# Performance work log

Measured on AMD Instinct MI355X. Metric: run time of the kernel, lower is better.

The kernel has to match this reference:

```python
import jax, jax.numpy as jnp
import numpy as np

D_MODEL = 1024
HEADS = 16
D_K = D_MODEL // HEADS
SCALE = 1.0 / np.sqrt(D_K)


def setup_inputs() -> dict:
    key = jax.random.key(0)
    ks = jax.random.split(key, 12)
    B, S = 4, 2048
    std = 1.0 / np.sqrt(D_MODEL)
    inp = {
        "query": jax.random.normal(ks[0], (B, S, D_MODEL), jnp.float32),
        "key": jax.random.normal(ks[1], (B, S, D_MODEL), jnp.float32),
        "value": jax.random.normal(ks[2], (B, S, D_MODEL), jnp.float32),
        # projection weights stored [in, out] (transpose of torch Linear)
        "Wq": jax.random.normal(ks[3], (D_MODEL, D_MODEL), jnp.float32) * std,
        "bq": jax.random.normal(ks[4], (D_MODEL,), jnp.float32) * std,
        "Wk": jax.random.normal(ks[5], (D_MODEL, D_MODEL), jnp.float32) * std,
        "bk": jax.random.normal(ks[6], (D_MODEL,), jnp.float32) * std,
        "Wv": jax.random.normal(ks[7], (D_MODEL, D_MODEL), jnp.float32) * std,
        "bv": jax.random.normal(ks[8], (D_MODEL,), jnp.float32) * std,
        "Wo": jax.random.normal(ks[9], (D_MODEL, D_MODEL), jnp.float32) * std,
        "bo": jax.random.normal(ks[10], (D_MODEL,), jnp.float32) * std,
    }
    return inp


def _proj(x, W, b):
    # [B,S,D] -> [B,S,H,Dk]
    B, S, _ = x.shape
    return (x @ W + b).reshape(B, S, HEADS, D_K)


def reference(query, key, value, Wq, bq, Wk, bk, Wv, bv, Wo, bo):
    B, S, _ = query.shape
    Q = _proj(query, Wq, bq)
    K = _proj(key, Wk, bk)
    V = _proj(value, Wv, bv)
    scores = jnp.einsum('bihd,bjhd->bijh', Q, K) * SCALE
    # FAITHFUL to original: nn.Softmax(dim=1) normalizes over the QUERY axis i
    attn = jax.nn.softmax(scores, axis=1)
    # dropout is identity at inference
    x = jnp.einsum('bijh,bjhd->bihd', attn, V).reshape(B, S, D_MODEL)
    return x @ Wo + bo
```

## Files before the change

### kernel.cpp

```cpp
#include <hip/hip_runtime.h>


#define B_   4
#define S_   2048
#define D_   1024
#define H_   16
#define DK_  64
#define BH_  64
#define SC2_    0.18033688f

typedef __bf16 bf16x2 __attribute__((ext_vector_type(2)));
typedef __bf16 bf16x4 __attribute__((ext_vector_type(4)));
typedef __bf16 bf16x8 __attribute__((ext_vector_type(8)));
typedef float  f32x4  __attribute__((ext_vector_type(4)));
typedef unsigned int u32;

#define MFMA16(a,b,c) __builtin_amdgcn_mfma_f32_16x16x32_bf16((a),(b),(c),0,0,0)

__device__ __forceinline__ bf16x8 ld8(const __bf16* p){ return *(const bf16x8*)p; }

__device__ __forceinline__ void gll16(const __bf16* g, __bf16* l) {
    __builtin_amdgcn_global_load_lds(
        (const __attribute__((address_space(1))) u32*)g,
        (__attribute__((address_space(3))) u32*)l, 16, 0, 0);
}

__global__ __launch_bounds__(256) void wtrans3(
    const float* __restrict__ W0, const float* __restrict__ W1,
    const float* __restrict__ W2, __bf16* __restrict__ Wt)
{
    __shared__ __align__(16) __bf16 Ls[64][80];
    const int t = threadIdx.x;
    const int k0 = blockIdx.x * 64, n0 = blockIdx.y * 64, z = blockIdx.z;
    const float* W = (z == 0) ? W0 : ((z == 1) ? W1 : W2);
    __bf16* out = Wt + (size_t)z * D_ * D_;

#pragma unroll
    for (int p = 0; p < 4; ++p) {
        int id = p*256 + t;
        int k = id >> 4, nq = id & 15;
        f32x4 v = *(const f32x4*)&W[(size_t)(k0 + k)*D_ + n0 + nq*4];
#pragma unroll
        for (int u = 0; u < 4; ++u) Ls[nq*4 + u][k] = (__bf16)v[u];
    }
    __syncthreads();
#pragma unroll
    for (int p = 0; p < 2; ++p) {
        int id = p*256 + t;
        int n = id >> 3, c = id & 7;
        *(bf16x8*)&out[(size_t)(n0 + n)*D_ + k0 + c*8] =
            *(const bf16x8*)&Ls[n][c*8];
    }
}

template<int ABF16, int MODE, int QS>
__global__ __launch_bounds__(256) void gemm128(
    const void* __restrict__ Ap, const __bf16* __restrict__ Wt,
    const float* __restrict__ bias, void* __restrict__ C)
{
    __shared__ __align__(16) __bf16 As[128*32];
    __shared__ __align__(16) __bf16 Bs[128*32];

    const int t = threadIdx.x, lane = t & 63, w = t >> 6;
    const int wm = w >> 1, wn = w & 1;
    const int fr = lane & 15, fq = lane >> 4;
    const int gid = blockIdx.x;
    const int m0 = (gid & 63) * 128, n0 = (gid >> 6) * 128;

    f32x4 acc[4][4];
#pragma unroll
    for (int i = 0; i < 4; ++i)
#pragma unroll
        for (int j = 0; j < 4; ++j) acc[i][j] = (f32x4){0.f,0.f,0.f,0.f};

    for (int kk = 0; kk < D_; kk += 32) {
        __syncthreads();
        if (ABF16) {
            const __bf16* Ab = (const __bf16*)Ap;
#pragma unroll
            for (int p = 0; p < 2; ++p) {
                int c = p*256 + t;
                int row = c >> 2, l = (c & 3) ^ (row & 3);
                gll16(&Ab[(size_t)(m0 + row)*D_ + kk + l*8],
                      &As[(size_t)(p*256 + (t & ~63))*8]);
            }
        } else {
            const float* Af = (const float*)Ap;
#pragma unroll
            for (int p = 0; p < 2; ++p) {
                int c = p*256 + t;
                int row = c >> 2, ch = c & 3;
                const float* ap = &Af[(size_t)(m0 + row)*D_ + kk + ch*8];
                f32x4 x0 = *(const f32x4*)ap;
                f32x4 x1 = *(const f32x4*)(ap + 4);
                bf16x8 v = { (__bf16)x0[0], (__bf16)x0[1], (__bf16)x0[2], (__bf16)x0[3],
                             (__bf16)x1[0], (__bf16)x1[1], (__bf16)x1[2], (__bf16)x1[3] };
                *(bf16x8*)&As[row*32 + 8*(ch ^ (row & 3))] = v;
            }
        }
#pragma unroll
        for (int p = 0; p < 2; ++p) {
            int c = p*256 + t;
            int n = c >> 2, l = (c & 3) ^ (n & 3);
            gll16(&Wt[(size_t)(n0 + n)*D_ + kk + l*8],
                  &Bs[(size_t)(p*256 + (t & ~63))*8]);
        }
        __syncthreads();

        bf16x8 af[4], bfr[4];
#pragma unroll
        for (int mt = 0; mt < 4; ++mt) {
            int row = wm*64 + mt*16 + fr;
            af[mt] = ld8(&As[row*32 + 8*(fq ^ (row & 3))]);
        }
#pragma unroll
        for (int nt = 0; nt < 4; ++nt) {
            int n = wn*64 + nt*16 + fr;
            bfr[nt] = ld8(&Bs[n*32 + 8*(fq ^ (n & 3))]);
        }
#pragma unroll
        for (int mt = 0; mt < 4; ++mt)
#pragma unroll
            for (int nt = 0; nt < 4; ++nt)
                acc[mt][nt] = MFMA16(af[mt], bfr[nt], acc[mt][nt]);
    }

#pragma unroll
    for (int mt = 0; mt < 4; ++mt)
#pragma unroll
        for (int nt = 0; nt < 4; ++nt) {
            int colg = n0 + wn*64 + nt*16 + fr;
            float bv = bias[colg];
#pragma unroll
            for (int r = 0; r < 4; ++r) {
                int rowg = m0 + wm*64 + mt*16 + fq*4 + r;
                float o = acc[mt][nt][r] + bv;
                if (QS) o *= SC2_;
                if (MODE == 0) {
                    ((float*)C)[(size_t)rowg*D_ + colg] = o;
                } else {
                    int b = rowg >> 11, sp = rowg & (S_-1);
                    int h = colg >> 6, dk = colg & 63;
                    ((__bf16*)C)[(((size_t)(b*H_ + h))*S_ + sp)*DK_ + dk] = (__bf16)o;
                }
            }
        }
}

__global__ __launch_bounds__(256) void colsum_rcp(
    const __bf16* __restrict__ Q, const __bf16* __restrict__ K,
    float* __restrict__ Rl)
{
    __shared__ __align__(16) __bf16 Qs[2][64*64];
    const int t = threadIdx.x, lane = t & 63, w = t >> 6;
    const int fr = lane & 15, fq = lane >> 4;
    const int gid = blockIdx.x;
    const int bh = gid & 63;
    const int jw = (gid >> 6)*128 + w*32;
    const __bf16* Qb = Q + (size_t)bh*S_*DK_;
    const __bf16* Kb = K + (size_t)bh*S_*DK_;

    bf16x8 kh[2][2];
#pragma unroll
    for (int jt = 0; jt < 2; ++jt) {
        const __bf16* kr = &Kb[(size_t)(jw + jt*16 + fr)*DK_];
        kh[jt][0] = ld8(kr + fq*8);
        kh[jt][1] = ld8(kr + 32 + fq*8);
    }

    float accl[2][4] = {};

#pragma unroll
    for (int p = 0; p < 2; ++p) {
        int c = p*256 + t;
        int i = c >> 3, l = (c & 7) ^ (i & 7);
        gll16(&Qb[(size_t)i*DK_ + l*8], &Qs[0][(size_t)(p*256 + (t & ~63))*8]);
    }
    __syncthreads();

    for (int i0 = 0; i0 < S_; i0 += 64) {
        const int cur = (i0 >> 6) & 1;
        if (i0 + 64 < S_) {
#pragma unroll
            for (int p = 0; p < 2; ++p) {
                int c = p*256 + t;
                int i = c >> 3, l = (c & 7) ^ (i & 7);
                gll16(&Qb[(size_t)(i0 + 64 + i)*DK_ + l*8],
                      &Qs[cur ^ 1][(size_t)(p*256 + (t & ~63))*8]);
            }
        }
#pragma unroll
        for (int it = 0; it < 4; ++it) {
            int i = it*16 + fr;
            bf16x8 q0 = ld8(&Qs[cur][i*64 + 8*(fq ^ (i & 7))]);
            bf16x8 q1 = ld8(&Qs[cur][i*64 + 8*((4 + fq) ^ (i & 7))]);
#pragma unroll
            for (int jt = 0; jt < 2; ++jt) {
                f32x4 s = MFMA16(kh[jt][0], q0, ((f32x4){0.f,0.f,0.f,0.f}));
                s = MFMA16(kh[jt][1], q1, s);
#pragma unroll
                for (int r = 0; r < 4; ++r)
                    accl[jt][r] += __builtin_amdgcn_exp2f(s[r]);
            }
        }
        __syncthreads();
    }
#pragma unroll
    for (int jt = 0; jt < 2; ++jt)
#pragma unroll
        for (int r = 0; r < 4; ++r) {
            accl[jt][r] += __shfl_xor(accl[jt][r], 1, 64);
            accl[jt][r] += __shfl_xor(accl[jt][r], 2, 64);
            accl[jt][r] += __shfl_xor(accl[jt][r], 4, 64);
            accl[jt][r] += __shfl_xor(accl[jt][r], 8, 64);
        }
    if (fr == 0) {
#pragma unroll
        for (int jt = 0; jt < 2; ++jt)
#pragma unroll
            for (int r = 0; r < 4; ++r)
                Rl[(size_t)bh*S_ + jw + jt*16 + fq*4 + r] = 1.0f / accl[jt][r];
    }
}

__global__ __launch_bounds__(512, 4) void attn_pv(
    const __bf16* __restrict__ Q, const __bf16* __restrict__ K,
    const __bf16* __restrict__ V, const float* __restrict__ Rl,
    __bf16* __restrict__ X)
{
    __shared__ __align__(16) __bf16 Ks[2][64*64];
    __shared__ __align__(16) __bf16 Vs[2][64*64];
    __shared__ __align__(16) __bf16 Pl[8][32*64];

    const int t = threadIdx.x, lane = t & 63, w = t >> 6;
    const int fr = lane & 15, fq = lane >> 4;
    const int gid = blockIdx.x;
    const int bh = gid & 63;
    const int iw = (gid >> 6)*256 + w*32;
    const __bf16* Qb = Q + (size_t)bh*S_*DK_;
    const __bf16* Kb = K + (size_t)bh*S_*DK_;
    const __bf16* Vb = V + (size_t)bh*S_*DK_;
    const float*  Rb = Rl + (size_t)bh*S_;

    bf16x8 qf[2][2];
#pragma unroll
    for (int it = 0; it < 2; ++it)
#pragma unroll
        for (int kf = 0; kf < 2; ++kf)
            qf[it][kf] = ld8(&Qb[(size_t)(iw + it*16 + fr)*DK_ + kf*32 + fq*8]);

    const int dq = t & 15, jp = t >> 4;
    const int krow = t >> 3;
    const int kchk = (t & 7) ^ (krow & 7);

    f32x4 acc[2][4];
#pragma unroll
    for (int it = 0; it < 2; ++it)
#pragma unroll
        for (int dt = 0; dt < 4; ++dt) acc[it][dt] = (f32x4){0.f,0.f,0.f,0.f};

    gll16(&Kb[(size_t)krow*DK_ + kchk*8], &Ks[0][(t & ~63)*8]);
    __syncthreads();

    for (int jg = 0; jg < S_; jg += 64) {
        const int cur = (jg >> 6) & 1;

        bf16x4 v0 = *(const bf16x4*)&Vb[(size_t)(jg + 2*jp    )*DK_ + dq*4];
        bf16x4 v1 = *(const bf16x4*)&Vb[(size_t)(jg + 2*jp + 1)*DK_ + dq*4];
        f32x4 rl[4];
#pragma unroll
        for (int jt = 0; jt < 4; ++jt)
            rl[jt] = *(const f32x4*)&Rb[jg + jt*16 + fq*4];
        if (jg + 64 < S_)
            gll16(&Kb[(size_t)(jg + 64 + krow)*DK_ + kchk*8],
                  &Ks[cur ^ 1][(t & ~63)*8]);

#pragma unroll
        for (int jt = 0; jt < 4; ++jt) {
            const __bf16* kb = &Ks[cur][(jt*16 + fr)*64];
            bf16x8 af0 = ld8(kb + ((fq    ) ^ (fr & 7))*8);
            bf16x8 af1 = ld8(kb + ((fq + 4) ^ (fr & 7))*8);
#pragma unroll
            for (int it = 0; it < 2; ++it) {
                f32x4 s = MFMA16(af0, qf[it][0], ((f32x4){0.f,0.f,0.f,0.f}));
                s = MFMA16(af1, qf[it][1], s);
                bf16x4 pv;
#pragma unroll
                for (int r = 0; r < 4; ++r)
                    pv[r] = (__bf16)(__builtin_amdgcn_exp2f(s[r]) * rl[jt][r]);
                int il = it*16 + fr;
                *(bf16x4*)&Pl[w][il*64 + (((jt*4 + fq) ^ (2*(fr & 7))))*4] = pv;
            }
        }

#pragma unroll
        for (int u = 0; u < 4; ++u) {
            int d = dq*4 + u;
            int f = (d ^ dq) & 7;
            *(bf16x2*)&Vs[cur][d*64 + (((jp >> 2) ^ f))*8 + (jp & 3)*2] =
                (bf16x2){ v0[u], v1[u] };
        }
        __syncthreads();

#pragma unroll
        for (int kh = 0; kh < 2; ++kh) {
            bf16x8 pa0 = ld8(&Pl[w][(     fr)*64 + (((fq + 4*kh) ^ (fr & 7)))*8]);
            bf16x8 pa1 = ld8(&Pl[w][(16 + fr)*64 + (((fq + 4*kh) ^ (fr & 7)))*8]);
#pragma unroll
            for (int dt = 0; dt < 4; ++dt) {
                int d = dt*16 + fr;
                int f = (d ^ (d >> 2)) & 7;
                bf16x8 vb = ld8(&Vs[cur][d*64 + (((kh*4 + fq) ^ f))*8]);
                acc[0][dt] = MFMA16(pa0, vb, acc[0][dt]);
                acc[1][dt] = MFMA16(pa1, vb, acc[1][dt]);
            }
        }
    }

    const int b = bh >> 4, h = bh & 15;
#pragma unroll
    for (int it = 0; it < 2; ++it)
#pragma unroll
        for (int dt = 0; dt < 4; ++dt)
#pragma unroll
            for (int r = 0; r < 4; ++r) {
                int i = iw + it*16 + fq*4 + r;
                X[((size_t)b*S_ + i)*D_ + h*DK_ + dt*16 + fr] =
                    (__bf16)acc[it][dt][r];
            }
}

extern "C" void kernel_launch(void* const* d_in, const int* in_sizes, int n_in,
                              void* d_out, int out_size, void* d_ws, size_t ws_size,
                              hipStream_t stream)
{
    const float* query = (const float*)d_in[0];
    const float* key   = (const float*)d_in[1];
    const float* value = (const float*)d_in[2];
    const float* Wq = (const float*)d_in[3];  const float* bq = (const float*)d_in[4];
    const float* Wk = (const float*)d_in[5];  const float* bk = (const float*)d_in[6];
    const float* Wv = (const float*)d_in[7];  const float* bv = (const float*)d_in[8];
    const float* Wo = (const float*)d_in[9];  const float* bo = (const float*)d_in[10];

    char* ws = (char*)d_ws;
    char* dob = (char*)d_out;
    const size_t MiB = 1024 * 1024;
    __bf16* Qb = (__bf16*)(ws);
    __bf16* Kb = (__bf16*)(ws + 16 * MiB);
    __bf16* Vb = (__bf16*)(ws + 32 * MiB);
    __bf16* Xb = (__bf16*)(ws + 48 * MiB);
    float*  Rlb = (float*)d_out;
    __bf16* Wt3 = (__bf16*)(dob + 1 * MiB);
    __bf16* WtO = (__bf16*)(ws);

    wtrans3<<<dim3(16,16,3), 256, 0, stream>>>(Wq, Wk, Wv, Wt3);

    gemm128<0,1,1><<<512, 256, 0, stream>>>(query, Wt3,                  bq, Qb);
    gemm128<0,1,0><<<512, 256, 0, stream>>>(key,   Wt3 + (size_t)D_*D_,  bk, Kb);
    gemm128<0,1,0><<<512, 256, 0, stream>>>(value, Wt3 + (size_t)2*D_*D_,bv, Vb);

    colsum_rcp<<<1024, 256, 0, stream>>>(Qb, Kb, Rlb);

    attn_pv<<<512, 512, 0, stream>>>(Qb, Kb, Vb, Rlb, Xb);

    wtrans3<<<dim3(16,16,1), 256, 0, stream>>>(Wo, Wo, Wo, WtO);

    gemm128<1,0,0><<<512, 256, 0, stream>>>(Xb, WtO, bo, d_out);
}
```

Before: 425.4 us.

## Double-buffer GEMM K tiles, fold softmax normalizer into MFMA accumulator init

The projection GEMM moves from a single-buffered 32-wide K step to a double-buffered 64-wide K step. The next tile's global loads are issued before the MFMAs on the current tile, so load latency overlaps compute and there are half as many barriers. The column-sum kernel now stores -log2 of the sum instead of its reciprocal. The attention kernel seeds the score MFMA accumulator with that value, which removes a per-element multiply after exp2. The PV MFMA block is also wrapped in raised wave priority. The cost is more LDS per block (64 KB), which may reduce GEMM occupancy, plus extra registers to hold the fp32 A prefetch.

New measurement: 373.5 us. 12.2% less time.

```diff
diff --git a/kernel.cpp b/kernel.cpp
--- a/kernel.cpp
+++ b/kernel.cpp
@@ -58,8 +58,8 @@
     const void* __restrict__ Ap, const __bf16* __restrict__ Wt,
     const float* __restrict__ bias, void* __restrict__ C)
 {
-    __shared__ __align__(16) __bf16 As[128*32];
-    __shared__ __align__(16) __bf16 Bs[128*32];
+    __shared__ __align__(16) __bf16 As[2][128*64];
+    __shared__ __align__(16) __bf16 Bs[2][128*64];
 
     const int t = threadIdx.x, lane = t & 63, w = t >> 6;
     const int wm = w >> 1, wn = w & 1;
@@ -67,63 +67,106 @@
     const int gid = blockIdx.x;
     const int m0 = (gid & 63) * 128, n0 = (gid >> 6) * 128;
 
+    const __bf16* Ab = (const __bf16*)Ap;
+    const float*  Af = (const float*)Ap;
+
     f32x4 acc[4][4];
 #pragma unroll
     for (int i = 0; i < 4; ++i)
 #pragma unroll
         for (int j = 0; j < 4; ++j) acc[i][j] = (f32x4){0.f,0.f,0.f,0.f};
 
-    for (int kk = 0; kk < D_; kk += 32) {
+#define STAGE_B(kk, bsel)                                                     \
+    _Pragma("unroll")                                                         \
+    for (int p = 0; p < 4; ++p) {                                             \
+        int idx = p*256 + t;                                                  \
+        int n = idx >> 3, l = (idx & 7) ^ (n & 7);                            \
+        gll16(&Wt[(size_t)(n0 + n)*D_ + (kk) + l*8],                          \
+              &Bs[bsel][(size_t)(p*256 + (t & ~63))*8]);                      \
+    }
+
+#define STAGE_A_BF(kk, bsel)                                                  \
+    _Pragma("unroll")                                                         \
+    for (int p = 0; p < 4; ++p) {                                             \
+        int idx = p*256 + t;                                                  \
+        int row = idx >> 3, l = (idx & 7) ^ (row & 7);                        \
+        gll16(&Ab[(size_t)(m0 + row)*D_ + (kk) + l*8],                        \
+              &As[bsel][(size_t)(p*256 + (t & ~63))*8]);                      \
+    }
+
+#define LOAD_A_F32(kk, xa)                                                    \
+    _Pragma("unroll")                                                         \
+    for (int p = 0; p < 4; ++p) {                                             \
+        int idx = p*256 + t;                                                  \
+        int row = idx >> 3, l = (idx & 7) ^ (row & 7);                        \
+        const float* ap = &Af[(size_t)(m0 + row)*D_ + (kk) + l*8];            \
+        xa[2*p]   = *(const f32x4*)ap;                                        \
+        xa[2*p+1] = *(const f32x4*)(ap + 4);                                  \
+    }
+
+#define WRITE_A_F32(xa, bsel)                                                 \
+    _Pragma("unroll")                                                         \
+    for (int p = 0; p < 4; ++p) {                                             \
+        f32x4 x0 = xa[2*p], x1 = xa[2*p+1];                                   \
+        bf16x8 v = { (__bf16)x0[0], (__bf16)x0[1], (__bf16)x0[2],             \
+                     (__bf16)x0[3], (__bf16)x1[0], (__bf16)x1[1],             \
+                     (__bf16)x1[2], (__bf16)x1[3] };                          \
+        *(bf16x8*)&As[bsel][(size_t)(p*256 + t)*8] = v;                       \
+    }
+
+    if (ABF16) {
+        STAGE_A_BF(0, 0)
+    } else {
+        f32x4 xa[8];
+        LOAD_A_F32(0, xa)
+        WRITE_A_F32(xa, 0)
+    }
+    STAGE_B(0, 0)
+    __syncthreads();
+
+    for (int kk = 0; kk < D_; kk += 64) {
+        const int cur = (kk >> 6) & 1;
+        const bool more = (kk + 64) < D_;
+
+        f32x4 xa[8];
+        if (more) {
+            if (ABF16) {
+                STAGE_A_BF(kk + 64, cur ^ 1)
+            } else {
+                LOAD_A_F32(kk + 64, xa)
+            }
+            STAGE_B(kk + 64, cur ^ 1)
+        }
+
+#pragma unroll
+        for (int kh = 0; kh < 2; ++kh) {
+            bf16x8 af[4], bfr[4];
+#pragma unroll
+            for (int mt = 0; mt < 4; ++mt) {
+                int row = wm*64 + mt*16 + fr;
+                af[mt] = ld8(&As[cur][row*64 + 8*((kh*4 + fq) ^ (row & 7))]);
+            }
+#pragma unroll
+            for (int nt = 0; nt < 4; ++nt) {
+                int n = wn*64 + nt*16 + fr;
+                bfr[nt] = ld8(&Bs[cur][n*64 + 8*((kh*4 + fq) ^ (n & 7))]);
+            }
+#pragma unroll
+            for (int mt = 0; mt < 4; ++mt)
+#pragma unroll
+                for (int nt = 0; nt < 4; ++nt)
+                    acc[mt][nt] = MFMA16(af[mt], bfr[nt], acc[mt][nt]);
+        }
+
+        if (more && !ABF16) {
+            WRITE_A_F32(xa, cur ^ 1)
+        }
         __syncthreads();
-        if (ABF16) {
-            const __bf16* Ab = (const __bf16*)Ap;
-#pragma unroll
-            for (int p = 0; p < 2; ++p) {
-                int c = p*256 + t;
-                int row = c >> 2, l = (c & 3) ^ (row & 3);
-                gll16(&Ab[(size_t)(m0 + row)*D_ + kk + l*8],
-                      &As[(size_t)(p*256 + (t & ~63))*8]);
-            }
-        } else {
-            const float* Af = (const float*)Ap;
-#pragma unroll
-            for (int p = 0; p < 2; ++p) {
-                int c = p*256 + t;
-                int row = c >> 2, ch = c & 3;
-                const float* ap = &Af[(size_t)(m0 + row)*D_ + kk + ch*8];
-                f32x4 x0 = *(const f32x4*)ap;
-                f32x4 x1 = *(const f32x4*)(ap + 4);
-                bf16x8 v = { (__bf16)x0[0], (__bf16)x0[1], (__bf16)x0[2], (__bf16)x0[3],
-                             (__bf16)x1[0], (__bf16)x1[1], (__bf16)x1[2], (__bf16)x1[3] };
-                *(bf16x8*)&As[row*32 + 8*(ch ^ (row & 3))] = v;
-            }
-        }
-#pragma unroll
-        for (int p = 0; p < 2; ++p) {
-            int c = p*256 + t;
-            int n = c >> 2, l = (c & 3) ^ (n & 3);
-            gll16(&Wt[(size_t)(n0 + n)*D_ + kk + l*8],
-                  &Bs[(size_t)(p*256 + (t & ~63))*8]);
-        }
-        __syncthreads();
-
-        bf16x8 af[4], bfr[4];
-#pragma unroll
-        for (int mt = 0; mt < 4; ++mt) {
-            int row = wm*64 + mt*16 + fr;
-            af[mt] = ld8(&As[row*32 + 8*(fq ^ (row & 3))]);
-        }
-#pragma unroll
-        for (int nt = 0; nt < 4; ++nt) {
-            int n = wn*64 + nt*16 + fr;
-            bfr[nt] = ld8(&Bs[n*32 + 8*(fq ^ (n & 3))]);
-        }
-#pragma unroll
-        for (int mt = 0; mt < 4; ++mt)
-#pragma unroll
-            for (int nt = 0; nt < 4; ++nt)
-                acc[mt][nt] = MFMA16(af[mt], bfr[nt], acc[mt][nt]);
-    }
+    }
+#undef STAGE_B
+#undef STAGE_A_BF
+#undef LOAD_A_F32
+#undef WRITE_A_F32
 
 #pragma unroll
     for (int mt = 0; mt < 4; ++mt)
@@ -149,7 +192,7 @@
 
 __global__ __launch_bounds__(256) void colsum_rcp(
     const __bf16* __restrict__ Q, const __bf16* __restrict__ K,
-    float* __restrict__ Rl)
+    float* __restrict__ Lg)
 {
     __shared__ __align__(16) __bf16 Qs[2][64*64];
     const int t = threadIdx.x, lane = t & 63, w = t >> 6;
@@ -219,13 +262,14 @@
         for (int jt = 0; jt < 2; ++jt)
 #pragma unroll
             for (int r = 0; r < 4; ++r)
-                Rl[(size_t)bh*S_ + jw + jt*16 + fq*4 + r] = 1.0f / accl[jt][r];
+                Lg[(size_t)bh*S_ + jw + jt*16 + fq*4 + r] =
+                    -__log2f(accl[jt][r]);
     }
 }
 
 __global__ __launch_bounds__(512, 4) void attn_pv(
     const __bf16* __restrict__ Q, const __bf16* __restrict__ K,
-    const __bf16* __restrict__ V, const float* __restrict__ Rl,
+    const __bf16* __restrict__ V, const float* __restrict__ Lg,
     __bf16* __restrict__ X)
 {
     __shared__ __align__(16) __bf16 Ks[2][64*64];
@@ -240,7 +284,7 @@
     const __bf16* Qb = Q + (size_t)bh*S_*DK_;
     const __bf16* Kb = K + (size_t)bh*S_*DK_;
     const __bf16* Vb = V + (size_t)bh*S_*DK_;
-    const float*  Rb = Rl + (size_t)bh*S_;
+    const float*  Rb = Lg + (size_t)bh*S_;
 
     bf16x8 qf[2][2];
 #pragma unroll
@@ -267,10 +311,10 @@
 
         bf16x4 v0 = *(const bf16x4*)&Vb[(size_t)(jg + 2*jp    )*DK_ + dq*4];
         bf16x4 v1 = *(const bf16x4*)&Vb[(size_t)(jg + 2*jp + 1)*DK_ + dq*4];
-        f32x4 rl[4];
+        f32x4 lg[4];
 #pragma unroll
         for (int jt = 0; jt < 4; ++jt)
-            rl[jt] = *(const f32x4*)&Rb[jg + jt*16 + fq*4];
+            lg[jt] = *(const f32x4*)&Rb[jg + jt*16 + fq*4];
         if (jg + 64 < S_)
             gll16(&Kb[(size_t)(jg + 64 + krow)*DK_ + kchk*8],
                   &Ks[cur ^ 1][(t & ~63)*8]);
@@ -282,12 +326,12 @@
             bf16x8 af1 = ld8(kb + ((fq + 4) ^ (fr & 7))*8);
 #pragma unroll
             for (int it = 0; it < 2; ++it) {
-                f32x4 s = MFMA16(af0, qf[it][0], ((f32x4){0.f,0.f,0.f,0.f}));
+                f32x4 s = MFMA16(af0, qf[it][0], lg[jt]);
                 s = MFMA16(af1, qf[it][1], s);
                 bf16x4 pv;
 #pragma unroll
                 for (int r = 0; r < 4; ++r)
-                    pv[r] = (__bf16)(__builtin_amdgcn_exp2f(s[r]) * rl[jt][r]);
+                    pv[r] = (__bf16)__builtin_amdgcn_exp2f(s[r]);
                 int il = it*16 + fr;
                 *(bf16x4*)&Pl[w][il*64 + (((jt*4 + fq) ^ (2*(fr & 7))))*4] = pv;
             }
@@ -302,6 +346,7 @@
         }
         __syncthreads();
 
+        __builtin_amdgcn_s_setprio(1);
 #pragma unroll
         for (int kh = 0; kh < 2; ++kh) {
             bf16x8 pa0 = ld8(&Pl[w][(     fr)*64 + (((fq + 4*kh) ^ (fr & 7)))*8]);
@@ -315,6 +360,7 @@
                 acc[1][dt] = MFMA16(pa1, vb, acc[1][dt]);
             }
         }
+        __builtin_amdgcn_s_setprio(0);
     }
 
     const int b = bh >> 4, h = bh & 15;
@@ -349,7 +395,7 @@
     __bf16* Kb = (__bf16*)(ws + 16 * MiB);
     __bf16* Vb = (__bf16*)(ws + 32 * MiB);
     __bf16* Xb = (__bf16*)(ws + 48 * MiB);
-    float*  Rlb = (float*)d_out;
+    float*  Lgb = (float*)d_out;
     __bf16* Wt3 = (__bf16*)(dob + 1 * MiB);
     __bf16* WtO = (__bf16*)(ws);
 
@@ -359,9 +405,9 @@
     gemm128<0,1,0><<<512, 256, 0, stream>>>(key,   Wt3 + (size_t)D_*D_,  bk, Kb);
     gemm128<0,1,0><<<512, 256, 0, stream>>>(value, Wt3 + (size_t)2*D_*D_,bv, Vb);
 
-    colsum_rcp<<<1024, 256, 0, stream>>>(Qb, Kb, Rlb);
-
-    attn_pv<<<512, 512, 0, stream>>>(Qb, Kb, Vb, Rlb, Xb);
+    colsum_rcp<<<1024, 256, 0, stream>>>(Qb, Kb, Lgb);
+
+    attn_pv<<<512, 512, 0, stream>>>(Qb, Kb, Vb, Lgb, Xb);
 
     wtrans3<<<dim3(16,16,1), 256, 0, stream>>>(Wo, Wo, Wo, WtO);
 
```
